# Performance work log

Measured on AMD Instinct MI355X. Metric: run time of the kernel, lower is better.

## Reference

```python
import jax, jax.numpy as jnp
import numpy as np

B, T, D, H = 4, 2048, 1024, 16
DK = D // H


def setup_inputs() -> dict:
    key = jax.random.key(0)
    ks = jax.random.split(key, 9)
    s = 1.0 / np.sqrt(D)
    x = jax.random.normal(ks[0], (B, T, D), dtype=jnp.float32)
    # causal mask: 1 = keep, 0 = masked (broadcastable over batch and heads)
    mask = jnp.tril(jnp.ones((T, T), dtype=jnp.int32))[None, None]
    params = {}
    for i, name in enumerate(['Wq', 'Wk', 'Wv', 'Wo']):
        params[name] = jax.random.normal(ks[1 + i], (D, D), dtype=jnp.float32) * s
    for i, name in enumerate(['bq', 'bk', 'bv', 'bo']):
        params[name] = jax.random.normal(ks[5 + i], (D,), dtype=jnp.float32) * s
    return {'x': x, 'mask': mask, **params}


def reference(x, mask, Wq, Wk, Wv, Wo, bq, bk, bv, bo):
    Bn, Tn, Dn = x.shape
    # torch.nn.Linear: y = x @ W.T + b
    q = (x @ Wq.T + bq).reshape(Bn, Tn, H, DK).transpose(0, 2, 1, 3)  # [B,H,T,dk]
    k = (x @ Wk.T + bk).reshape(Bn, Tn, H, DK).transpose(0, 2, 1, 3)
    v = (x @ Wv.T + bv).reshape(Bn, Tn, H, DK).transpose(0, 2, 1, 3)
    scores = jnp.einsum('bhqd,bhkd->bhqk', q, k) / jnp.sqrt(jnp.float32(DK))
    scores = jnp.where(mask == 0, -jnp.inf, scores)
    attn = jax.nn.softmax(scores, axis=-1)
    out = jnp.einsum('bhqk,bhkd->bhqd', attn, v)  # [B,H,T,dk]
    out = out.transpose(0, 2, 1, 3).reshape(Bn, Tn, Dn)
    return out @ Wo.T + bo
```

## Files before the change

### kernel.cpp

```cpp
#include <hip/hip_runtime.h>
#include <hip/hip_bf16.h>

#define T_LEN 2048
#define D_DIM 1024
#define H_NUM 16
#define DK 64

typedef unsigned short u16;
typedef __bf16 bf16x8 __attribute__((ext_vector_type(8)));
typedef float f32x4 __attribute__((ext_vector_type(4)));
typedef u16 u16x8 __attribute__((ext_vector_type(8)));
typedef u16 u16x4 __attribute__((ext_vector_type(4)));

#define AS1 __attribute__((address_space(1)))
#define AS3 __attribute__((address_space(3)))

#define QSCALE 0.18033688011112042f

__device__ __forceinline__ u16 f2bf(float f) {
    unsigned u = __builtin_bit_cast(unsigned, f);
    unsigned rounding = 0x7FFFu + ((u >> 16) & 1u);
    return (u16)((u + rounding) >> 16);
}

__global__ __launch_bounds__(256) void cvt_bf16(const float* __restrict__ in,
                                                u16* __restrict__ out, int n8) {
    int i = blockIdx.x * blockDim.x + threadIdx.x;
    if (i >= n8) return;
    const float4* p = (const float4*)in + (size_t)i * 2;
    float4 a = p[0], b = p[1];
    u16x8 r;
    r[0] = f2bf(a.x); r[1] = f2bf(a.y); r[2] = f2bf(a.z); r[3] = f2bf(a.w);
    r[4] = f2bf(b.x); r[5] = f2bf(b.y); r[6] = f2bf(b.z); r[7] = f2bf(b.w);
    *((u16x8*)out + i) = r;
}

__global__ __launch_bounds__(256) void cvt4_bf16(const float* __restrict__ a,
                                                 const float* __restrict__ b,
                                                 const float* __restrict__ c,
                                                 const float* __restrict__ d,
                                                 u16* __restrict__ out, int n8per) {
    int s = blockIdx.y;
    const float* src = s == 0 ? a : (s == 1 ? b : (s == 2 ? c : d));
    int i = blockIdx.x * blockDim.x + threadIdx.x;
    if (i >= n8per) return;
    const float4* p = (const float4*)src + (size_t)i * 2;
    float4 x = p[0], y = p[1];
    u16x8 r;
    r[0] = f2bf(x.x); r[1] = f2bf(x.y); r[2] = f2bf(x.z); r[3] = f2bf(x.w);
    r[4] = f2bf(y.x); r[5] = f2bf(y.y); r[6] = f2bf(y.z); r[7] = f2bf(y.w);
    *((u16x8*)(out + (size_t)s * n8per * 8) + i) = r;
}

template <int MODE>
__global__ __launch_bounds__(256) void gemm_bt(const u16* __restrict__ A,
                                               const u16* __restrict__ W,
                                               const float* __restrict__ b0,
                                               const float* __restrict__ b1,
                                               const float* __restrict__ b2,
                                               void* __restrict__ Cout,
                                               int M, int N, int K,
                                               int nxt, int nyt) {
    __shared__ u16 lA[2][128 * 32];
    __shared__ u16 lB[2][128 * 32];
    const int tid = threadIdx.x;
    const int w = tid >> 6, lane = tid & 63;

    const int bid = blockIdx.x;
    const int idx = bid >> 3;
    const int y = idx % nyt;
    const int x = (bid & 7) * (nxt >> 3) + idx / nyt;
    const int tm = x * 128;
    const int tn = y * 128;

    const int wm = (w >> 1) * 64, wn = (w & 1) * 64;
    const int kgrp = (lane >> 4) * 8;

    f32x4 acc[4][4] = {};

    auto stage = [&](int buf, int k0) {
#pragma unroll
        for (int r = 0; r < 2; ++r) {
            int c = r * 256 + tid;
            int row = c >> 2, col = (c & 3) * 8;
            __builtin_amdgcn_global_load_lds(
                (AS1 const void*)(A + (size_t)(tm + row) * K + k0 + col),
                (AS3 void*)(&lA[buf][(r * 256 + w * 64) * 8]), 16, 0, 0);
            __builtin_amdgcn_global_load_lds(
                (AS1 const void*)(W + (size_t)(tn + row) * K + k0 + col),
                (AS3 void*)(&lB[buf][(r * 256 + w * 64) * 8]), 16, 0, 0);
        }
    };

    stage(0, 0);
    asm volatile("s_waitcnt vmcnt(0)" ::: "memory");
    __syncthreads();

    const int niter = K >> 5;
    for (int it = 0; it < niter; ++it) {
        const int cur = it & 1;
        if (it + 1 < niter) stage(cur ^ 1, (it + 1) << 5);

        bf16x8 af[4], bfr[4];
#pragma unroll
        for (int i = 0; i < 4; ++i) {
            af[i]  = *(const bf16x8*)(&lA[cur][(wm + i * 16 + (lane & 15)) * 32 + kgrp]);
            bfr[i] = *(const bf16x8*)(&lB[cur][(wn + i * 16 + (lane & 15)) * 32 + kgrp]);
        }
#pragma unroll
        for (int mi = 0; mi < 4; ++mi)
#pragma unroll
            for (int ni = 0; ni < 4; ++ni)
                acc[mi][ni] = __builtin_amdgcn_mfma_f32_16x16x32_bf16(
                    af[mi], bfr[ni], acc[mi][ni], 0, 0, 0);

        asm volatile("s_waitcnt vmcnt(0)" ::: "memory");
        __syncthreads();
    }

    const int mtx = tn >> 10;
    const float* bp = mtx == 0 ? b0 : (mtx == 1 ? b1 : b2);
    const int crow0 = (lane >> 4) * 4;
    const int ccol = lane & 15;
#pragma unroll
    for (int mi = 0; mi < 4; ++mi) {
#pragma unroll
        for (int ni = 0; ni < 4; ++ni) {
            int n = tn + wn + ni * 16 + ccol;
            float bv = bp[n & 1023];
#pragma unroll
            for (int r = 0; r < 4; ++r) {
                int m = tm + wm + mi * 16 + crow0 + r;
                float val = acc[mi][ni][r] + bv;
                if (MODE == 0) {
                    ((float*)Cout)[(size_t)m * N + n] = val;
                } else {
                    if (mtx == 0) val *= QSCALE;
                    int b = m >> 11, t = m & (T_LEN - 1);
                    int nn = n & 1023;
                    int h = nn >> 6, d = nn & 63;
                    ((u16*)Cout)[(size_t)mtx * 8388608 +
                                 ((size_t)(b * H_NUM + h) * T_LEN + t) * DK + d] = f2bf(val);
                }
            }
        }
    }
}

__global__ __launch_bounds__(512) void attn_fwd(const u16* __restrict__ q,
                                                const u16* __restrict__ k,
                                                const u16* __restrict__ v,
                                                u16* __restrict__ o) {
    __shared__ u16 lK[2][64 * 64];
    __shared__ u16 lV[2][64 * 64];
    __shared__ u16 lP[8][16 * 64];

    const int tid = threadIdx.x, w = tid >> 6, lane = tid & 63;
    const int bid = blockIdx.x;
    const int idx = bid >> 3;
    const int bh = (bid & 7) * 8 + (idx & 7);
    const int bx = idx >> 3;

    const u16* qb = q + (size_t)bh * T_LEN * DK;
    const u16* kb = k + (size_t)bh * T_LEN * DK;
    const u16* vb = v + (size_t)bh * T_LEN * DK;

    const int g = lane >> 4;
    const int ccol = lane & 15;
    const int kg = tid >> 4;
    const int dc = tid & 15;
    const int wk = w - 4;
    const int b_ = bh >> 4, h_ = bh & 15;

    for (int seg = 0; seg < 2; ++seg) {
        const int qblk = seg ? (15 - bx) : bx;
        const int q0 = qblk * 128;
        const int ntiles = 2 * qblk + 2;
        const int rowbase = q0 + w * 16;

        bf16x8 qa[2];
#pragma unroll
        for (int kk = 0; kk < 2; ++kk)
            qa[kk] = *(const bf16x8*)(qb + (size_t)(rowbase + ccol) * DK + kk * 32 + g * 8);

        f32x4 oacc[4] = {};
        float mrow[4], lpart[4];
#pragma unroll
        for (int r = 0; r < 4; ++r) { mrow[r] = -1e30f; lpart[r] = 0.f; }

        u16x4 vr[4];
        if (w >= 4) {
#pragma unroll
            for (int r2 = 0; r2 < 2; ++r2) {
                int c = r2 * 256 + wk * 64 + lane;
                int row = c >> 3, ch = c & 7;
                __builtin_amdgcn_global_load_lds(
                    (AS1 const void*)(kb + (size_t)row * DK + (ch ^ (row & 7)) * 8),
                    (AS3 void*)(&lK[0][(r2 * 256 + wk * 64) * 8]), 16, 0, 0);
            }
        } else {
#pragma unroll
            for (int i = 0; i < 4; ++i)
                vr[i] = *(const u16x4*)(vb + (size_t)(kg * 4 + i) * DK + dc * 4);
        }

        for (int kt = 0; kt < ntiles; ++kt) {
            const int bf = kt & 1;
            const int kv0 = kt << 6;
            asm volatile("s_waitcnt vmcnt(0)" ::: "memory");
            if (w < 4) {
#pragma unroll
                for (int j = 0; j < 4; ++j) {
                    int d = dc * 4 + j;
                    u16x4 t4;
                    t4[0] = vr[0][j]; t4[1] = vr[1][j]; t4[2] = vr[2][j]; t4[3] = vr[3][j];
                    *(u16x4*)(&lV[bf][d * 64 +
                        (((kg >> 1) ^ ((d >> 1) & 7)) * 8 + (kg & 1) * 4)]) = t4;
                }
            }
            __syncthreads();

            if (kt + 1 < ntiles) {
                const int kvn = (kt + 1) << 6;
                if (w >= 4) {
#pragma unroll
                    for (int r2 = 0; r2 < 2; ++r2) {
                        int c = r2 * 256 + wk * 64 + lane;
                        int row = c >> 3, ch = c & 7;
                        __builtin_amdgcn_global_load_lds(
                            (AS1 const void*)(kb + (size_t)(kvn + row) * DK + (ch ^ (row & 7)) * 8),
                            (AS3 void*)(&lK[bf ^ 1][(r2 * 256 + wk * 64) * 8]), 16, 0, 0);
                    }
                } else {
#pragma unroll
                    for (int i = 0; i < 4; ++i)
                        vr[i] = *(const u16x4*)(vb + (size_t)(kvn + kg * 4 + i) * DK + dc * 4);
                }
            }

            if (kv0 < rowbase + 16) {
                f32x4 sacc[4] = {};
#pragma unroll
                for (int nt = 0; nt < 4; ++nt)
#pragma unroll
                    for (int kk = 0; kk < 2; ++kk) {
                        bf16x8 kf = *(const bf16x8*)(&lK[bf][(nt * 16 + ccol) * 64 +
                                                     (((kk * 4 + g) ^ (ccol & 7)) * 8)]);
                        sacc[nt] = __builtin_amdgcn_mfma_f32_16x16x32_bf16(
                            qa[kk], kf, sacc[nt], 0, 0, 0);
                    }

                const bool full = (kv0 + 63) <= rowbase;
                float p[4][4], scal[4];
                bool anyresc = false;
#pragma unroll
                for (int r = 0; r < 4; ++r) {
                    int grow = rowbase + g * 4 + r;
                    float s[4], mx = -1e30f;
#pragma unroll
                    for (int nt = 0; nt < 4; ++nt) {
                        float sv = sacc[nt][r];
                        if (!full && (kv0 + nt * 16 + ccol > grow)) sv = -1e30f;
                        s[nt] = sv;
                        mx = fmaxf(mx, sv);
                    }
#pragma unroll
                    for (int off = 8; off; off >>= 1) mx = fmaxf(mx, __shfl_xor(mx, off));
                    const bool skiprow = (mx <= mrow[r] + 8.f);
                    float mnew = skiprow ? mrow[r] : mx;
                    float rsl = 0.f;
#pragma unroll
                    for (int nt = 0; nt < 4; ++nt) {
                        p[nt][r] = __builtin_amdgcn_exp2f(s[nt] - mnew);
                        rsl += p[nt][r];
                    }
                    scal[r] = skiprow ? 1.f : __builtin_amdgcn_exp2f(mrow[r] - mnew);
                    anyresc |= !skiprow;
                    lpart[r] = lpart[r] * scal[r] + rsl;
                    mrow[r] = mnew;
                }
                if (__any(anyresc)) {
#pragma unroll
                    for (int nt2 = 0; nt2 < 4; ++nt2)
#pragma unroll
                        for (int r = 0; r < 4; ++r) oacc[nt2][r] *= scal[r];
                }

#pragma unroll
                for (int nt = 0; nt < 4; ++nt)
#pragma unroll
                    for (int r = 0; r < 4; ++r) {
                        int qrow = g * 4 + r;
                        int swzq = ((qrow ^ (qrow >> 3)) & 7) * 8;
                        lP[w][qrow * 64 + ((nt * 16 + ccol) ^ swzq)] = f2bf(p[nt][r]);
                    }
                asm volatile("s_waitcnt lgkmcnt(0)" ::: "memory");
                bf16x8 pa[2];
                {
                    int swzr = (ccol ^ (ccol >> 3)) & 7;
#pragma unroll
                    for (int kk2 = 0; kk2 < 2; ++kk2)
                        pa[kk2] = *(const bf16x8*)(&lP[w][ccol * 64 +
                                                   ((kk2 * 4 + g) ^ swzr) * 8]);
                }
                const int vsw = (ccol >> 1) & 7;
#pragma unroll
                for (int nt2 = 0; nt2 < 4; ++nt2) {
#pragma unroll
                    for (int kk2 = 0; kk2 < 2; ++kk2) {
                        bf16x8 vf = *(const bf16x8*)(&lV[bf][(nt2 * 16 + ccol) * 64 +
                                                     (((kk2 * 4 + g) ^ vsw) * 8)]);
                        oacc[nt2] = __builtin_amdgcn_mfma_f32_16x16x32_bf16(
                            pa[kk2], vf, oacc[nt2], 0, 0, 0);
                    }
                }
            }
        }
        __syncthreads();

#pragma unroll
        for (int r = 0; r < 4; ++r) {
            float rs = lpart[r];
#pragma unroll
            for (int off = 8; off; off >>= 1) rs += __shfl_xor(rs, off);
            float inv = 1.0f / rs;
            int trow = rowbase + g * 4 + r;
#pragma unroll
            for (int nt2 = 0; nt2 < 4; ++nt2) {
                float val = oacc[nt2][r] * inv;
                o[(size_t)(b_ * T_LEN + trow) * D_DIM + h_ * DK + nt2 * 16 + ccol] = f2bf(val);
            }
        }
    }
}

extern "C" void kernel_launch(void* const* d_in, const int* in_sizes, int n_in,
                              void* d_out, int out_size, void* d_ws, size_t ws_size,
                              hipStream_t stream) {
    const float* x  = (const float*)d_in[0];
    const float* Wq = (const float*)d_in[2];
    const float* Wk = (const float*)d_in[3];
    const float* Wv = (const float*)d_in[4];
    const float* Wo = (const float*)d_in[5];
    const float* bq = (const float*)d_in[6];
    const float* bk = (const float*)d_in[7];
    const float* bv = (const float*)d_in[8];
    const float* bo = (const float*)d_in[9];

    char* ws = (char*)d_ws;
    u16* xb   = (u16*)(ws);
    u16* wqb  = (u16*)(ws + 16777216);
    u16* wob  = (u16*)(ws + 23068672);
    u16* qws  = (u16*)(ws + 25165824);
    u16* kws  = (u16*)(ws + 41943040);
    u16* vws  = (u16*)(ws + 58720256);
    u16* attnb = xb;

    cvt_bf16<<<4096, 256, 0, stream>>>(x, xb, 1048576);
    cvt4_bf16<<<dim3(512, 4), 256, 0, stream>>>(Wq, Wk, Wv, Wo, wqb, 131072);

    gemm_bt<1><<<1536, 256, 0, stream>>>(xb, wqb, bq, bk, bv, qws, 8192, 3072, 1024, 64, 24);

    attn_fwd<<<512, 512, 0, stream>>>(qws, kws, vws, attnb);

    gemm_bt<0><<<512, 256, 0, stream>>>(attnb, wob, bo, bo, bo, d_out, 8192, 1024, 1024, 64, 8);
}
```

Measured before the change: 330.5 us.

## Compute transposed QK^T so each lane owns a query row for softmax

Swaps the MFMA operands for S so each lane holds a single query column's scores. Softmax max and sum then need only two cross-lane shuffles per tile instead of four per row, with one running max and sum per lane. P is written as packed 4-element vectors into a padded LDS buffer, and rescale factors are passed through a small LDS array so they line up with the O accumulator layout. It also adds s_setprio around the MFMA blocks, at the cost of extra LDS traffic and an added barrier per segment.

```diff
diff --git a/kernel.cpp b/kernel.cpp
--- a/kernel.cpp
+++ b/kernel.cpp
@@ -153,7 +153,8 @@
                                                 u16* __restrict__ o) {
     __shared__ u16 lK[2][64 * 64];
     __shared__ u16 lV[2][64 * 64];
-    __shared__ u16 lP[8][16 * 64];
+    __shared__ u16 lP[8][16 * 72];
+    __shared__ float lSc[8][16];
 
     const int tid = threadIdx.x, w = tid >> 6, lane = tid & 63;
     const int bid = blockIdx.x;
@@ -177,6 +178,7 @@
         const int q0 = qblk * 128;
         const int ntiles = 2 * qblk + 2;
         const int rowbase = q0 + w * 16;
+        const int myq = rowbase + ccol;
 
         bf16x8 qa[2];
 #pragma unroll
@@ -184,9 +186,7 @@
             qa[kk] = *(const bf16x8*)(qb + (size_t)(rowbase + ccol) * DK + kk * 32 + g * 8);
 
         f32x4 oacc[4] = {};
-        float mrow[4], lpart[4];
-#pragma unroll
-        for (int r = 0; r < 4; ++r) { mrow[r] = -1e30f; lpart[r] = 0.f; }
+        float mrow = -1e30f, lpart = 0.f;
 
         u16x4 vr[4];
         if (w >= 4) {
@@ -240,6 +240,7 @@
 
             if (kv0 < rowbase + 16) {
                 f32x4 sacc[4] = {};
+                __builtin_amdgcn_s_setprio(1);
 #pragma unroll
                 for (int nt = 0; nt < 4; ++nt)
 #pragma unroll
@@ -247,63 +248,65 @@
                         bf16x8 kf = *(const bf16x8*)(&lK[bf][(nt * 16 + ccol) * 64 +
                                                      (((kk * 4 + g) ^ (ccol & 7)) * 8)]);
                         sacc[nt] = __builtin_amdgcn_mfma_f32_16x16x32_bf16(
-                            qa[kk], kf, sacc[nt], 0, 0, 0);
-                    }
+                            kf, qa[kk], sacc[nt], 0, 0, 0);
+                    }
+                __builtin_amdgcn_s_setprio(0);
 
                 const bool full = (kv0 + 63) <= rowbase;
-                float p[4][4], scal[4];
-                bool anyresc = false;
-#pragma unroll
-                for (int r = 0; r < 4; ++r) {
-                    int grow = rowbase + g * 4 + r;
-                    float s[4], mx = -1e30f;
-#pragma unroll
-                    for (int nt = 0; nt < 4; ++nt) {
+                float mx = -1e30f;
+#pragma unroll
+                for (int nt = 0; nt < 4; ++nt)
+#pragma unroll
+                    for (int r = 0; r < 4; ++r) {
                         float sv = sacc[nt][r];
-                        if (!full && (kv0 + nt * 16 + ccol > grow)) sv = -1e30f;
-                        s[nt] = sv;
+                        if (!full && (kv0 + nt * 16 + g * 4 + r > myq)) sv = -1e30f;
+                        sacc[nt][r] = sv;
                         mx = fmaxf(mx, sv);
                     }
-#pragma unroll
-                    for (int off = 8; off; off >>= 1) mx = fmaxf(mx, __shfl_xor(mx, off));
-                    const bool skiprow = (mx <= mrow[r] + 8.f);
-                    float mnew = skiprow ? mrow[r] : mx;
-                    float rsl = 0.f;
-#pragma unroll
-                    for (int nt = 0; nt < 4; ++nt) {
-                        p[nt][r] = __builtin_amdgcn_exp2f(s[nt] - mnew);
-                        rsl += p[nt][r];
-                    }
-                    scal[r] = skiprow ? 1.f : __builtin_amdgcn_exp2f(mrow[r] - mnew);
-                    anyresc |= !skiprow;
-                    lpart[r] = lpart[r] * scal[r] + rsl;
-                    mrow[r] = mnew;
-                }
-                if (__any(anyresc)) {
+                mx = fmaxf(mx, __shfl_xor(mx, 16));
+                mx = fmaxf(mx, __shfl_xor(mx, 32));
+
+                const bool skiprow = (mx <= mrow + 8.f);
+                float mnew = skiprow ? mrow : mx;
+                float p[4][4];
+                float rsl = 0.f;
+#pragma unroll
+                for (int nt = 0; nt < 4; ++nt)
+#pragma unroll
+                    for (int r = 0; r < 4; ++r) {
+                        float pv = __builtin_amdgcn_exp2f(sacc[nt][r] - mnew);
+                        p[nt][r] = pv;
+                        rsl += pv;
+                    }
+                float scal = skiprow ? 1.f : __builtin_amdgcn_exp2f(mrow - mnew);
+                lpart = lpart * scal + rsl;
+                mrow = mnew;
+
+                if (lane < 16) lSc[w][lane] = scal;
+#pragma unroll
+                for (int nt = 0; nt < 4; ++nt) {
+                    u16x4 t4;
+                    t4[0] = f2bf(p[nt][0]); t4[1] = f2bf(p[nt][1]);
+                    t4[2] = f2bf(p[nt][2]); t4[3] = f2bf(p[nt][3]);
+                    *(u16x4*)(&lP[w][ccol * 72 + nt * 16 + g * 4]) = t4;
+                }
+                asm volatile("s_waitcnt lgkmcnt(0)" ::: "memory");
+
+                f32x4 scalC = *(const f32x4*)(&lSc[w][g * 4]);
+                if (__any(!skiprow)) {
 #pragma unroll
                     for (int nt2 = 0; nt2 < 4; ++nt2)
 #pragma unroll
-                        for (int r = 0; r < 4; ++r) oacc[nt2][r] *= scal[r];
-                }
-
-#pragma unroll
-                for (int nt = 0; nt < 4; ++nt)
-#pragma unroll
-                    for (int r = 0; r < 4; ++r) {
-                        int qrow = g * 4 + r;
-                        int swzq = ((qrow ^ (qrow >> 3)) & 7) * 8;
-                        lP[w][qrow * 64 + ((nt * 16 + ccol) ^ swzq)] = f2bf(p[nt][r]);
-                    }
-                asm volatile("s_waitcnt lgkmcnt(0)" ::: "memory");
+                        for (int r = 0; r < 4; ++r) oacc[nt2][r] *= scalC[r];
+                }
+
                 bf16x8 pa[2];
-                {
-                    int swzr = (ccol ^ (ccol >> 3)) & 7;
-#pragma unroll
-                    for (int kk2 = 0; kk2 < 2; ++kk2)
-                        pa[kk2] = *(const bf16x8*)(&lP[w][ccol * 64 +
-                                                   ((kk2 * 4 + g) ^ swzr) * 8]);
-                }
+#pragma unroll
+                for (int kk2 = 0; kk2 < 2; ++kk2)
+                    pa[kk2] = *(const bf16x8*)(&lP[w][ccol * 72 + kk2 * 32 + g * 8]);
+
                 const int vsw = (ccol >> 1) & 7;
+                __builtin_amdgcn_s_setprio(1);
 #pragma unroll
                 for (int nt2 = 0; nt2 < 4; ++nt2) {
 #pragma unroll
@@ -314,16 +317,20 @@
                             pa[kk2], vf, oacc[nt2], 0, 0, 0);
                     }
                 }
+                __builtin_amdgcn_s_setprio(0);
             }
         }
         __syncthreads();
 
+        float rs = lpart;
+        rs += __shfl_xor(rs, 16);
+        rs += __shfl_xor(rs, 32);
+        if (lane < 16) lSc[w][lane] = rs;
+        asm volatile("s_waitcnt lgkmcnt(0)" ::: "memory");
+        f32x4 rsC = *(const f32x4*)(&lSc[w][g * 4]);
 #pragma unroll
         for (int r = 0; r < 4; ++r) {
-            float rs = lpart[r];
-#pragma unroll
-            for (int off = 8; off; off >>= 1) rs += __shfl_xor(rs, off);
-            float inv = 1.0f / rs;
+            float inv = 1.0f / rsC[r];
             int trow = rowbase + g * 4 + r;
 #pragma unroll
             for (int nt2 = 0; nt2 < 4; ++nt2) {
@@ -331,6 +338,7 @@
                 o[(size_t)(b_ * T_LEN + trow) * D_DIM + h_ * DK + nt2 * 16 + ccol] = f2bf(val);
             }
         }
+        __syncthreads();
     }
 }
 
```

Measured after the change: 291.8 us. 1.13x faster.
